# Kernel optimization log

Hardware: AMD Instinct MI355X
Metric: run time of the kernel (lower is better)

## Reference

```python
import jax, jax.numpy as jnp
import numpy as np

B, S, E, H = 2, 2048, 1024, 16
HD = E // H  # 64
NEG = -1e24


def setup_inputs() -> dict:
    key = jax.random.key(0)
    ks = jax.random.split(key, 20)
    sc_e = 1.0 / np.sqrt(E)
    inp = {
        "q_matrix": jax.random.normal(ks[0], (B, S, E), jnp.float32),
        "k_matrix": jax.random.normal(ks[1], (B, S, E), jnp.float32),
        "v_matrix": jax.random.normal(ks[2], (B, S, E), jnp.float32),
        "mask": jax.random.randint(ks[3], (B, S, S), 0, 2).astype(bool),
        # global QKV projections (embed_dim -> embed_dim)
        "Wq": jax.random.normal(ks[4], (E, E), jnp.float32) * sc_e,
        "bq": jnp.zeros((E,), jnp.float32),
        "Wk": jax.random.normal(ks[5], (E, E), jnp.float32) * sc_e,
        "bk": jnp.zeros((E,), jnp.float32),
        "Wv": jax.random.normal(ks[6], (E, E), jnp.float32) * sc_e,
        "bv": jnp.zeros((E,), jnp.float32),
        # per-head QKV projections (embed_dim -> head_dim), batched over heads
        "Whq": jax.random.normal(ks[7], (H, E, HD), jnp.float32) * sc_e,
        "bhq": jnp.zeros((H, HD), jnp.float32),
        "Whk": jax.random.normal(ks[8], (H, E, HD), jnp.float32) * sc_e,
        "bhk": jnp.zeros((H, HD), jnp.float32),
        "Whv": jax.random.normal(ks[9], (H, E, HD), jnp.float32) * sc_e,
        "bhv": jnp.zeros((H, HD), jnp.float32),
        # output projection
        "Wo": jax.random.normal(ks[10], (E, E), jnp.float32) * sc_e,
        "bo": jnp.zeros((E,), jnp.float32),
    }
    return inp


def reference(q_matrix, k_matrix, v_matrix, mask, Wq, bq, Wk, bk, Wv, bv,
              Whq, bhq, Whk, bhk, Whv, bhv, Wo, bo):
    # global projections [B,S,E]
    qg = q_matrix @ Wq + bq
    kg = k_matrix @ Wk + bk
    vg = v_matrix @ Wv + bv
    # per-head projections -> [B,H,S,HD]
    qh = jnp.einsum('bse,hed->bhsd', qg, Whq) + bhq[None, :, None, :]
    kh = jnp.einsum('bse,hed->bhsd', kg, Whk) + bhk[None, :, None, :]
    vh = jnp.einsum('bse,hed->bhsd', vg, Whv) + bhv[None, :, None, :]
    # scaled dot-product attention, scores [B,H,S,S]
    scores = jnp.einsum('bhsd,bhtd->bhst', qh, kh) / jnp.sqrt(jnp.float32(HD))
    scores = jnp.where(mask[:, None, :, :], NEG, scores)
    weights = jax.nn.softmax(scores, axis=-1)
    out = jnp.einsum('bhst,bhtd->bhsd', weights, vh)
    # concat heads (head order along last dim, matching torch.cat)
    x = out.transpose(0, 2, 1, 3).reshape(out.shape[0], out.shape[2], E)
    return x @ Wo + bo
```

## Files before the change

### kernel.cpp

```cpp
#include <hip/hip_runtime.h>
#include <hip/hip_bf16.h>

typedef unsigned short us16;
typedef __attribute__((ext_vector_type(8))) short short8;
typedef __attribute__((ext_vector_type(4))) float float4v;

#define E_DIM 1024
#define S_LEN 2048
#define B_DIM 2
#define H_DIM 16
#define HD_DIM 64
#define M_ROWS 4096
#define SCALE2 0.18033688011112042f

__device__ __forceinline__ float b2f(us16 b) {
    return __uint_as_float(((unsigned int)b) << 16);
}
__device__ __forceinline__ us16 f2b(float f) {
    unsigned int u = __float_as_uint(f);
    unsigned int r = (u + 0x7fffu + ((u >> 16) & 1u)) >> 16;
    return (us16)r;
}

__device__ __forceinline__ void gload16(const us16* g, us16* lds_uniform_base) {
    __builtin_amdgcn_global_load_lds(
        (const __attribute__((address_space(1))) void*)g,
        (__attribute__((address_space(3))) void*)lds_uniform_base, 16, 0, 0);
}

__global__ __launch_bounds__(256) void prep(
    const float* __restrict__ q, const float* __restrict__ k, const float* __restrict__ v,
    const float* __restrict__ Wq, const float* __restrict__ Wk, const float* __restrict__ Wv,
    const float* __restrict__ Whq, const float* __restrict__ Whk, const float* __restrict__ Whv,
    const float* __restrict__ Wo,
    const float* __restrict__ bq, const float* __restrict__ bk, const float* __restrict__ bv,
    const float* __restrict__ bhq, const float* __restrict__ bhk, const float* __restrict__ bhv,
    const int* __restrict__ mask,
    us16* qb, us16* kb, us16* vb, us16* Wqb, us16* Wkb, us16* Wvb,
    us16* WhqT, us16* WhkT, us16* WhvT, us16* WoT,
    us16* marr,
    float* bcq, float* bck, float* bcv, float* zbias)
{
    __shared__ us16 tile[32][33];
    __shared__ float red[4][64];
    int blk = blockIdx.x, tid = threadIdx.x;

    if (blk < 7680) {
        const float* in; us16* out; int idx;
        if (blk < 6144) {
            int z = blk >> 11, rem = blk & 2047;
            in = z == 0 ? q : z == 1 ? k : v;
            out = z == 0 ? qb : z == 1 ? kb : vb;
            idx = (rem * 256 + tid) * 8;
        } else {
            int t = blk - 6144, z = t >> 9, rem = t & 511;
            in = z == 0 ? Wq : z == 1 ? Wk : Wv;
            out = z == 0 ? Wqb : z == 1 ? Wkb : Wvb;
            idx = (rem * 256 + tid) * 8;
        }
        float4 f0 = *(const float4*)(in + idx);
        float4 f1 = *(const float4*)(in + idx + 4);
        us16 t8[8] = {f2b(f0.x), f2b(f0.y), f2b(f0.z), f2b(f0.w),
                      f2b(f1.x), f2b(f1.y), f2b(f1.z), f2b(f1.w)};
        *(uint4*)(out + idx) = *(const uint4*)t8;
    } else if (blk < 11776) {
        int t = blk - 7680, z = t >> 10, rem = t & 1023;
        const float* in = z == 0 ? Whq : z == 1 ? Whk : z == 2 ? Whv : Wo;
        us16* out = z == 0 ? WhqT : z == 1 ? WhkT : z == 2 ? WhvT : WoT;
        int mode = (z < 3) ? 1 : 0;
        int bx = rem & 31, by = rem >> 5;
        int tx = tid & 31, ty = tid >> 5;
#pragma unroll
        for (int i = 0; i < 4; ++i) {
            int e = by * 32 + ty + i * 8;
            int c = bx * 32 + tx;
            size_t src;
            if (mode == 0) src = (size_t)e * E_DIM + c;
            else           src = ((size_t)(c >> 6) * E_DIM + e) * 64 + (c & 63);
            tile[ty + i * 8][tx] = f2b(in[src]);
        }
        __syncthreads();
#pragma unroll
        for (int i = 0; i < 4; ++i) {
            int c = bx * 32 + ty + i * 8;
            int e = by * 32 + tx;
            out[(size_t)c * E_DIM + e] = tile[tx][ty + i * 8];
        }
    } else if (blk < 15872) {
        int g = (blk - 11776) * 256 + tid;
        int lane = g & 63, ld = (g >> 6) & 1, wv = (g >> 7) & 7;
        int q0t = (g >> 10) & 15, ktz = (g >> 14) & 31, bb = g >> 19;
        int quad = lane >> 4, l16 = lane & 15;
        int qq = q0t * 128 + wv * 16 + l16;
        int t0 = ktz * 64 + ld * 32 + quad * 4;
        const int* mp = mask + ((size_t)bb * S_LEN + qq) * S_LEN + t0;
        int4 ma = *(const int4*)mp;
        int4 mb2 = *(const int4*)(mp + 16);
        const us16 NEGB = f2b(-1e38f);
        us16 t8[8];
        t8[0] = ma.x ? NEGB : (us16)0;  t8[1] = ma.y ? NEGB : (us16)0;
        t8[2] = ma.z ? NEGB : (us16)0;  t8[3] = ma.w ? NEGB : (us16)0;
        t8[4] = mb2.x ? NEGB : (us16)0; t8[5] = mb2.y ? NEGB : (us16)0;
        t8[6] = mb2.z ? NEGB : (us16)0; t8[7] = mb2.w ? NEGB : (us16)0;
        *(uint4*)&marr[(size_t)g * 8] = *(const uint4*)t8;
    } else if (blk < 15920) {
        int t = blk - 15872, z = t >> 4, h = t & 15;
        const float* bg = z == 0 ? bq : z == 1 ? bk : bv;
        const float* Wh = z == 0 ? Whq : z == 1 ? Whk : Whv;
        const float* bh = z == 0 ? bhq : z == 1 ? bhk : bhv;
        float* bc = z == 0 ? bcq : z == 1 ? bck : bcv;
        float sc = (z == 0) ? SCALE2 : 1.0f;
        int d = tid & 63, part = tid >> 6;
        float acc = 0.f;
        int j0 = part * 256;
        for (int j = j0; j < j0 + 256; ++j)
            acc += bg[j] * Wh[((size_t)h * E_DIM + j) * HD_DIM + d];
        red[part][d] = acc;
        __syncthreads();
        if (tid < 64)
            bc[h * 64 + tid] = (red[0][tid] + red[1][tid] + red[2][tid] + red[3][tid] + bh[h * 64 + tid]) * sc;
    } else {
        int i = (blk - 15920) * 256 + tid;
        if (i < 1024) zbias[i] = 0.f;
    }
}

#define BK 32

__device__ __forceinline__ void gemm_body(
    const us16* __restrict__ A, const us16* __restrict__ Bt,
    const float* __restrict__ bias, void* __restrict__ Cp,
    int M, int N, int K, int bxt, int byt, int omode)
{
    __shared__ us16 As[128 * BK];
    __shared__ us16 Bs[128 * BK];

    int tid = threadIdx.x;
    int wave = tid >> 6, lane = tid & 63;
    int quad = lane >> 4, l16 = lane & 15;
    int wm = (wave >> 1) * 64, wn = (wave & 1) * 64;
    int bm0 = byt * 128, bn0 = bxt * 128;
    int srow = lane >> 2;
    int gcol = (((lane & 3) ^ (srow & 3)) << 3);
    int rslot = ((quad ^ (l16 & 3)) << 3);

    float4v acc[4][4];
#pragma unroll
    for (int i = 0; i < 4; ++i)
#pragma unroll
        for (int j = 0; j < 4; ++j)
#pragma unroll
            for (int r = 0; r < 4; ++r) acc[i][j][r] = 0.f;

    for (int k0 = 0; k0 < K; k0 += BK) {
#pragma unroll
        for (int c = 0; c < 2; ++c) {
            int r0 = 32 * wave + 16 * c;
            gload16(A  + (size_t)(bm0 + r0 + srow) * K + k0 + gcol, &As[r0 * BK]);
            gload16(Bt + (size_t)(bn0 + r0 + srow) * K + k0 + gcol, &Bs[r0 * BK]);
        }
        __syncthreads();
        short8 af[4], bfr[4];
#pragma unroll
        for (int i = 0; i < 4; ++i)
            af[i] = *(const short8*)&As[(wm + i * 16 + l16) * BK + rslot];
#pragma unroll
        for (int j = 0; j < 4; ++j)
            bfr[j] = *(const short8*)&Bs[(wn + j * 16 + l16) * BK + rslot];
#pragma unroll
        for (int i = 0; i < 4; ++i)
#pragma unroll
            for (int j = 0; j < 4; ++j)
                acc[i][j] = __builtin_amdgcn_mfma_f32_16x16x32_bf16(af[i], bfr[j], acc[i][j], 0, 0, 0);
        __syncthreads();
    }

#pragma unroll
    for (int i = 0; i < 4; ++i) {
#pragma unroll
        for (int j = 0; j < 4; ++j) {
#pragma unroll
            for (int r = 0; r < 4; ++r) {
                int row = bm0 + wm + i * 16 + quad * 4 + r;
                int col = bn0 + wn + j * 16 + l16;
                float vv = acc[i][j][r] + ((omode == 3) ? bias[row] : bias[col]);
                if (omode == 1) {
                    int b = row >> 11, s = row & 2047, h = col >> 6, d = col & 63;
                    ((us16*)Cp)[(((size_t)(b * H_DIM + h) * S_LEN + s) * HD_DIM) + d] = f2b(vv);
                } else {
                    int h = row >> 6, d = row & 63, b = col >> 11, sl = col & 2047;
                    ((us16*)Cp)[(((size_t)(b * H_DIM + h) * HD_DIM + d) * S_LEN) + sl] = f2b(vv);
                }
            }
        }
    }
}

__global__ __launch_bounds__(256) void proj_all(
    const us16* __restrict__ qb, const us16* __restrict__ kb, const us16* __restrict__ vb,
    const us16* __restrict__ WcqT, const us16* __restrict__ WckT, const us16* __restrict__ WcvT,
    const float* __restrict__ bcq, const float* __restrict__ bck, const float* __restrict__ bcv,
    us16* __restrict__ qhb, us16* __restrict__ khb, us16* __restrict__ vtb)
{
    int bx = blockIdx.x;
    int z = bx >> 8, t = bx & 255;
    if (z == 0)      gemm_body(qb, WcqT, bcq, qhb, M_ROWS, E_DIM, E_DIM, t & 7, t >> 3, 1);
    else if (z == 1) gemm_body(kb, WckT, bck, khb, M_ROWS, E_DIM, E_DIM, t & 7, t >> 3, 1);
    else             gemm_body(WcvT, vb, bcv, vtb, E_DIM, M_ROWS, E_DIM, t & 31, t >> 5, 3);
}

template<int OMODE>
__device__ __forceinline__ void gemm64_body(
    const us16* __restrict__ A, const us16* __restrict__ Bt,
    const float* __restrict__ bias, void* __restrict__ Cp,
    int M, int N, int K, int bxt, int byt, float oscale)
{
    __shared__ us16 As[64 * BK];
    __shared__ us16 Bs[128 * BK];

    int tid = threadIdx.x;
    int wave = tid >> 6, lane = tid & 63;
    int quad = lane >> 4, l16 = lane & 15;
    int wm = (wave >> 1) * 32, wn = (wave & 1) * 64;
    int bm0 = byt * 64, bn0 = bxt * 128;
    int srow = lane >> 2;
    int gcol = (((lane & 3) ^ (srow & 3)) << 3);
    int rslot = ((quad ^ (l16 & 3)) << 3);

    float4v acc[2][4];
#pragma unroll
    for (int i = 0; i < 2; ++i)
#pragma unroll
        for (int j = 0; j < 4; ++j)
#pragma unroll
            for (int r = 0; r < 4; ++r) acc[i][j][r] = 0.f;

    for (int k0 = 0; k0 < K; k0 += BK) {
        gload16(A + (size_t)(bm0 + 16 * wave + srow) * K + k0 + gcol, &As[16 * wave * BK]);
#pragma unroll
        for (int c = 0; c < 2; ++c) {
            int r0 = 32 * wave + 16 * c;
            gload16(Bt + (size_t)(bn0 + r0 + srow) * K + k0 + gcol, &Bs[r0 * BK]);
        }
        __syncthreads();
        short8 af[2], bfr[4];
#pragma unroll
        for (int i = 0; i < 2; ++i)
            af[i] = *(const short8*)&As[(wm + i * 16 + l16) * BK + rslot];
#pragma unroll
        for (int j = 0; j < 4; ++j)
            bfr[j] = *(const short8*)&Bs[(wn + j * 16 + l16) * BK + rslot];
#pragma unroll
        for (int i = 0; i < 2; ++i)
#pragma unroll
            for (int j = 0; j < 4; ++j)
                acc[i][j] = __builtin_amdgcn_mfma_f32_16x16x32_bf16(af[i], bfr[j], acc[i][j], 0, 0, 0);
        __syncthreads();
    }

#pragma unroll
    for (int i = 0; i < 2; ++i)
#pragma unroll
        for (int j = 0; j < 4; ++j)
#pragma unroll
            for (int r = 0; r < 4; ++r) {
                int row = bm0 + wm + i * 16 + quad * 4 + r;
                int col = bn0 + wn + j * 16 + l16;
                float vv = (acc[i][j][r] + bias[col]) * oscale;
                if (OMODE == 0) ((us16*)Cp)[(size_t)row * N + col] = f2b(vv);
                else            ((float*)Cp)[(size_t)row * N + col] = vv;
            }
}

__global__ __launch_bounds__(256) void wgemm3(
    const us16* A0, const us16* A1, const us16* A2,
    const us16* B0, const us16* B1, const us16* B2,
    const float* zbias, us16* C0, us16* C1, us16* C2)
{
    int z = blockIdx.z;
    const us16* A = z == 0 ? A0 : z == 1 ? A1 : A2;
    const us16* Bt = z == 0 ? B0 : z == 1 ? B1 : B2;
    us16* C = z == 0 ? C0 : z == 1 ? C1 : C2;
    float sc = (z == 0) ? SCALE2 : 1.0f;
    gemm64_body<0>(A, Bt, zbias, C, E_DIM, E_DIM, E_DIM, blockIdx.x, blockIdx.y, sc);
}

__global__ __launch_bounds__(256) void gemm_out64(
    const us16* __restrict__ A, const us16* __restrict__ Bt,
    const float* __restrict__ bias, float* __restrict__ C, int M, int N, int K)
{
    gemm64_body<2>(A, Bt, bias, C, M, N, K, blockIdx.x, blockIdx.y, 1.0f);
}

#define PST 72
#define NT 32

__global__ __launch_bounds__(512) void attn_kernel(
    const us16* __restrict__ qh, const us16* __restrict__ kh,
    const us16* __restrict__ vt, const us16* __restrict__ marr,
    us16* __restrict__ x)
{
    __shared__ us16 Ks[2][64 * 64];
    __shared__ us16 Vs[2][64 * 64];
    __shared__ us16 Pw[8][16 * PST];

    int tid = threadIdx.x;
    int w = tid >> 6, lane = tid & 63;
    int quad = lane >> 4, l16 = lane & 15;

    int wg = blockIdx.x;
    int xcd = wg & 7, idx = wg >> 3;
    int bh = xcd * 4 + (idx >> 4);
    int q0t = idx & 15;
    int q0 = q0t * 128;
    int b = bh >> 4;
    const size_t base = (size_t)bh * (S_LEN * HD_DIM);

    int qrow = q0 + w * 16 + l16;
    short8 qf0, qf1;
    {
        const us16* qp = qh + base + (size_t)qrow * HD_DIM + quad * 8;
        qf0 = *(const short8*)qp;
        qf1 = *(const short8*)(qp + 32);
    }

    short8 onesf;
#pragma unroll
    for (int j = 0; j < 8; ++j) onesf[j] = (short)0x3F80;

    int strow = w * 8 + (lane >> 3);
    int scol = ((lane & 7) ^ (strow & 7)) * 8;
    const us16* ksrc0 = kh + base + (size_t)strow * HD_DIM + scol;
    const us16* vsrc0 = vt + base + (size_t)strow * S_LEN + scol;

    const us16* mb0p = marr + ((((size_t)(b * 32) * 16 + q0t) * 8 + w) * 1024)
                            + (size_t)lane * 8;

    int slotA = (quad ^ (l16 & 7)) * 8;
    int slotB = slotA ^ 32;

    float4v o[4];
#pragma unroll
    for (int dt = 0; dt < 4; ++dt)
#pragma unroll
        for (int r = 0; r < 4; ++r) o[dt][r] = 0.f;
    float4v o_l;
#pragma unroll
    for (int r = 0; r < 4; ++r) o_l[r] = 0.f;

    auto QK = [&](const us16* KsC, uint4 m0, uint4 m1, float4v* sc) {
        __builtin_amdgcn_s_setprio(1);
#pragma unroll
        for (int ct = 0; ct < 4; ++ct) {
            int tt = ct * 16 + l16;
            short8 kf0 = *(const short8*)&KsC[tt * 64 + slotA];
            short8 kf1 = *(const short8*)&KsC[tt * 64 + slotB];
            unsigned w0, w1;
            if (ct == 0)      { w0 = m0.x; w1 = m0.y; }
            else if (ct == 1) { w0 = m0.z; w1 = m0.w; }
            else if (ct == 2) { w0 = m1.x; w1 = m1.y; }
            else              { w0 = m1.z; w1 = m1.w; }
            float4v a;
            a[0] = __uint_as_float(w0 << 16);
            a[1] = __uint_as_float(w0 & 0xFFFF0000u);
            a[2] = __uint_as_float(w1 << 16);
            a[3] = __uint_as_float(w1 & 0xFFFF0000u);
            a = __builtin_amdgcn_mfma_f32_16x16x32_bf16(kf0, qf0, a, 0, 0, 0);
            a = __builtin_amdgcn_mfma_f32_16x16x32_bf16(kf1, qf1, a, 0, 0, 0);
            sc[ct] = a;
        }
        __builtin_amdgcn_s_setprio(0);
    };

    gload16(ksrc0, &Ks[0][w * 512]);
    gload16(vsrc0, &Vs[0][w * 512]);
    gload16(ksrc0 + (size_t)64 * HD_DIM, &Ks[1][w * 512]);
    gload16(vsrc0 + 64, &Vs[1][w * 512]);
    uint4 mc0 = *(const uint4*)(mb0p);
    uint4 mc1 = *(const uint4*)(mb0p + 512);
    asm volatile("s_waitcnt vmcnt(2)" ::: "memory");
    __builtin_amdgcn_s_barrier();
    __builtin_amdgcn_sched_barrier(0);

    float4v sc[4];
    QK(Ks[0], mc0, mc1, sc);

    for (int t = 0; t < NT; ++t) {
        int cur = t & 1;

        uint4 mn0 = mc0, mn1 = mc1;
        if (t + 1 < NT) {
            const us16* mp = mb0p + (size_t)(t + 1) * 131072;
            mn0 = *(const uint4*)(mp);
            mn1 = *(const uint4*)(mp + 512);
        }

#pragma unroll
        for (int ct = 0; ct < 4; ++ct) {
            float p0 = __builtin_amdgcn_exp2f(sc[ct][0]);
            float p1 = __builtin_amdgcn_exp2f(sc[ct][1]);
            float p2 = __builtin_amdgcn_exp2f(sc[ct][2]);
            float p3 = __builtin_amdgcn_exp2f(sc[ct][3]);
            uint2 pk;
            asm("v_cvt_pk_bf16_f32 %0, %1, %2" : "=v"(pk.x) : "v"(p0), "v"(p1));
            asm("v_cvt_pk_bf16_f32 %0, %1, %2" : "=v"(pk.y) : "v"(p2), "v"(p3));
            *(uint2*)&Pw[w][l16 * PST + ct * 16 + quad * 4] = pk;
        }

        short8 pf0 = *(const short8*)&Pw[w][l16 * PST + quad * 8];
        short8 pf1 = *(const short8*)&Pw[w][l16 * PST + 32 + quad * 8];
        const us16* VsC = Vs[cur];
        __builtin_amdgcn_s_setprio(1);
#pragma unroll
        for (int dt = 0; dt < 4; ++dt) {
            int d = dt * 16 + l16;
            short8 vf0 = *(const short8*)&VsC[d * 64 + slotA];
            short8 vf1 = *(const short8*)&VsC[d * 64 + slotB];
            o[dt] = __builtin_amdgcn_mfma_f32_16x16x32_bf16(pf0, vf0, o[dt], 0, 0, 0);
            o[dt] = __builtin_amdgcn_mfma_f32_16x16x32_bf16(pf1, vf1, o[dt], 0, 0, 0);
        }
        o_l = __builtin_amdgcn_mfma_f32_16x16x32_bf16(pf0, onesf, o_l, 0, 0, 0);
        o_l = __builtin_amdgcn_mfma_f32_16x16x32_bf16(pf1, onesf, o_l, 0, 0, 0);
        __builtin_amdgcn_s_setprio(0);

        if (t + 1 == NT) break;

        __builtin_amdgcn_s_barrier();
        __builtin_amdgcn_sched_barrier(0);

        if (t + 2 < NT) {
            gload16(ksrc0 + (size_t)((t + 2) * 64) * HD_DIM, &Ks[cur][w * 512]);
            gload16(vsrc0 + (t + 2) * 64, &Vs[cur][w * 512]);
            asm volatile("s_waitcnt vmcnt(2)" ::: "memory");
        } else {
            asm volatile("s_waitcnt vmcnt(0)" ::: "memory");
        }
        __builtin_amdgcn_s_barrier();
        __builtin_amdgcn_sched_barrier(0);

        mc0 = mn0; mc1 = mn1;
        QK(Ks[cur ^ 1], mc0, mc1, sc);
    }

    float linv[4];
#pragma unroll
    for (int r = 0; r < 4; ++r) linv[r] = 1.0f / o_l[r];
    int h = bh & 15;
    int srow0 = q0 + w * 16 + quad * 4;
#pragma unroll
    for (int r = 0; r < 4; ++r) {
        size_t xro = ((size_t)(b * S_LEN + srow0 + r)) * E_DIM + h * HD_DIM;
#pragma unroll
        for (int dt = 0; dt < 4; ++dt)
            x[xro + dt * 16 + l16] = f2b(o[dt][r] * linv[r]);
    }
}

extern "C" void kernel_launch(void* const* d_in, const int* in_sizes, int n_in,
                              void* d_out, int out_size, void* d_ws, size_t ws_size,
                              hipStream_t stream) {
    const float* q    = (const float*)d_in[0];
    const float* k    = (const float*)d_in[1];
    const float* v    = (const float*)d_in[2];
    const int*   mask = (const int*)d_in[3];
    const float* Wq = (const float*)d_in[4];   const float* bq = (const float*)d_in[5];
    const float* Wk = (const float*)d_in[6];   const float* bk = (const float*)d_in[7];
    const float* Wv = (const float*)d_in[8];   const float* bv = (const float*)d_in[9];
    const float* Whq = (const float*)d_in[10]; const float* bhq = (const float*)d_in[11];
    const float* Whk = (const float*)d_in[12]; const float* bhk = (const float*)d_in[13];
    const float* Whv = (const float*)d_in[14]; const float* bhv = (const float*)d_in[15];
    const float* Wo = (const float*)d_in[16];  const float* bo = (const float*)d_in[17];

    us16* ws = (us16*)d_ws;
    const size_t M1 = (size_t)1 << 20;
    us16* WhqT = ws + 0 * M1;
    us16* WhkT = ws + 1 * M1;
    us16* WhvT = ws + 2 * M1;
    us16* WoT  = ws + 3 * M1;
    us16* WcqT = ws + 4 * M1;
    us16* WckT = ws + 5 * M1;
    us16* WcvT = ws + 6 * M1;
    us16* Wqb  = ws + 7 * M1;
    us16* Wkb  = ws + 8 * M1;
    us16* Wvb  = ws + 9 * M1;
    us16* qb   = ws + 10 * M1;
    us16* kb   = ws + 14 * M1;
    us16* vb   = ws + 18 * M1;
    us16* qhb  = ws + 22 * M1;
    us16* khb  = ws + 26 * M1;
    us16* vtb  = ws + 30 * M1;
    us16* xb   = vb;
    float* bcq   = (float*)(ws + 34 * M1);
    float* bck   = bcq + 1024;
    float* bcv   = bck + 1024;
    float* zbias = bcv + 1024;
    us16*  marr  = ws + 35 * M1;

    prep<<<15924, 256, 0, stream>>>(q, k, v, Wq, Wk, Wv, Whq, Whk, Whv, Wo,
                                    bq, bk, bv, bhq, bhk, bhv, mask,
                                    qb, kb, vb, Wqb, Wkb, Wvb,
                                    WhqT, WhkT, WhvT, WoT, marr,
                                    bcq, bck, bcv, zbias);

    wgemm3<<<dim3(8, 16, 3), 256, 0, stream>>>(WhqT, WhkT, WhvT, Wqb, Wkb, Wvb, zbias,
                                               WcqT, WckT, WcvT);

    proj_all<<<768, 256, 0, stream>>>(qb, kb, vb, WcqT, WckT, WcvT,
                                      bcq, bck, bcv, qhb, khb, vtb);

    attn_kernel<<<512, 512, 0, stream>>>(qhb, khb, vtb, marr, xb);

    gemm_out64<<<dim3(8, 64), 256, 0, stream>>>(xb, WoT, bo, (float*)d_out,
                                                M_ROWS, E_DIM, E_DIM);
}
```

Baseline: 298.3 us.

## Stage mask conversion through LDS for coalesced reads; use 128x128 GEMM tiles everywhere

The mask-to-bf16 conversion now reads 128x64 mask tiles row-contiguously into shared memory, then shuffles them into the MFMA-fragment layout before writing. The old version read scattered 16-byte pieces per lane directly from global memory. Separately, the 64-row GEMM body is removed, and the weight-combine and output-projection GEMMs now use the 128x128 tiled body, which halves their grids. Larger tiles give more reuse per block but fewer blocks for occupancy, and the prep kernel's shared-memory footprint grows.

```diff
diff --git a/kernel.cpp b/kernel.cpp
--- a/kernel.cpp
+++ b/kernel.cpp
@@ -43,6 +43,7 @@
 {
     __shared__ us16 tile[32][33];
     __shared__ float red[4][64];
+    __shared__ us16 Lm[128][72];
     int blk = blockIdx.x, tid = threadIdx.x;
 
     if (blk < 7680) {
@@ -86,25 +87,49 @@
             int e = by * 32 + tx;
             out[(size_t)c * E_DIM + e] = tile[tx][ty + i * 8];
         }
-    } else if (blk < 15872) {
-        int g = (blk - 11776) * 256 + tid;
-        int lane = g & 63, ld = (g >> 6) & 1, wv = (g >> 7) & 7;
-        int q0t = (g >> 10) & 15, ktz = (g >> 14) & 31, bb = g >> 19;
-        int quad = lane >> 4, l16 = lane & 15;
-        int qq = q0t * 128 + wv * 16 + l16;
-        int t0 = ktz * 64 + ld * 32 + quad * 4;
-        const int* mp = mask + ((size_t)bb * S_LEN + qq) * S_LEN + t0;
-        int4 ma = *(const int4*)mp;
-        int4 mb2 = *(const int4*)(mp + 16);
+    } else if (blk < 12032) {
+        int t2 = blk - 11776;
+        int ktg = t2 & 7, q0t2 = (t2 >> 3) & 15, bb = t2 >> 7;
         const us16 NEGB = f2b(-1e38f);
-        us16 t8[8];
-        t8[0] = ma.x ? NEGB : (us16)0;  t8[1] = ma.y ? NEGB : (us16)0;
-        t8[2] = ma.z ? NEGB : (us16)0;  t8[3] = ma.w ? NEGB : (us16)0;
-        t8[4] = mb2.x ? NEGB : (us16)0; t8[5] = mb2.y ? NEGB : (us16)0;
-        t8[6] = mb2.z ? NEGB : (us16)0; t8[7] = mb2.w ? NEGB : (us16)0;
-        *(uint4*)&marr[(size_t)g * 8] = *(const uint4*)t8;
-    } else if (blk < 15920) {
-        int t = blk - 15872, z = t >> 4, h = t & 15;
+        for (int kk = 0; kk < 4; ++kk) {
+            int kt = ktg * 4 + kk;
+            __syncthreads();
+#pragma unroll
+            for (int sgi = 0; sgi < 2; ++sgi) {
+                int seg = tid * 2 + sgi;
+                int row = seg >> 2, part = seg & 3;
+                const int* mp = mask + ((size_t)bb * S_LEN + q0t2 * 128 + row) * S_LEN
+                                + kt * 64 + part * 16;
+                us16 tmp[16];
+#pragma unroll
+                for (int gi = 0; gi < 4; ++gi) {
+                    int4 mv = *(const int4*)(mp + gi * 4);
+                    tmp[gi * 4 + 0] = mv.x ? NEGB : (us16)0;
+                    tmp[gi * 4 + 1] = mv.y ? NEGB : (us16)0;
+                    tmp[gi * 4 + 2] = mv.z ? NEGB : (us16)0;
+                    tmp[gi * 4 + 3] = mv.w ? NEGB : (us16)0;
+                }
+                *(uint4*)&Lm[row][part * 16]     = *(const uint4*)&tmp[0];
+                *(uint4*)&Lm[row][part * 16 + 8] = *(const uint4*)&tmp[8];
+            }
+            __syncthreads();
+            int wv2 = tid >> 5, ld2 = (tid >> 4) & 1, lb = (tid & 15) * 4;
+            us16 obuf[32];
+#pragma unroll
+            for (int li = 0; li < 4; ++li) {
+                int lane2 = lb + li;
+                int row = wv2 * 16 + (lane2 & 15);
+                int tb = ld2 * 32 + (lane2 >> 4) * 4;
+                *(uint2*)&obuf[li * 8]     = *(const uint2*)&Lm[row][tb];
+                *(uint2*)&obuf[li * 8 + 4] = *(const uint2*)&Lm[row][tb + 16];
+            }
+            size_t gbase = (((size_t)(bb * 32 + kt) * 16 + q0t2) * 8192) + (size_t)tid * 32;
+#pragma unroll
+            for (int gi = 0; gi < 4; ++gi)
+                *(uint4*)&marr[gbase + gi * 8] = *(const uint4*)&obuf[gi * 8];
+        }
+    } else if (blk < 12080) {
+        int t = blk - 12032, z = t >> 4, h = t & 15;
         const float* bg = z == 0 ? bq : z == 1 ? bk : bv;
         const float* Wh = z == 0 ? Whq : z == 1 ? Whk : Whv;
         const float* bh = z == 0 ? bhq : z == 1 ? bhk : bhv;
@@ -120,7 +145,7 @@
         if (tid < 64)
             bc[h * 64 + tid] = (red[0][tid] + red[1][tid] + red[2][tid] + red[3][tid] + bh[h * 64 + tid]) * sc;
     } else {
-        int i = (blk - 15920) * 256 + tid;
+        int i = (blk - 12080) * 256 + tid;
         if (i < 1024) zbias[i] = 0.f;
     }
 }
@@ -130,7 +155,7 @@
 __device__ __forceinline__ void gemm_body(
     const us16* __restrict__ A, const us16* __restrict__ Bt,
     const float* __restrict__ bias, void* __restrict__ Cp,
-    int M, int N, int K, int bxt, int byt, int omode)
+    int M, int N, int K, int bxt, int byt, int omode, float oscale)
 {
     __shared__ us16 As[128 * BK];
     __shared__ us16 Bs[128 * BK];
@@ -184,9 +209,13 @@
                 int row = bm0 + wm + i * 16 + quad * 4 + r;
                 int col = bn0 + wn + j * 16 + l16;
                 float vv = acc[i][j][r] + ((omode == 3) ? bias[row] : bias[col]);
-                if (omode == 1) {
+                if (omode == 0) {
+                    ((us16*)Cp)[(size_t)row * N + col] = f2b(vv * oscale);
+                } else if (omode == 1) {
                     int b = row >> 11, s = row & 2047, h = col >> 6, d = col & 63;
                     ((us16*)Cp)[(((size_t)(b * H_DIM + h) * S_LEN + s) * HD_DIM) + d] = f2b(vv);
+                } else if (omode == 2) {
+                    ((float*)Cp)[(size_t)row * N + col] = vv;
                 } else {
                     int h = row >> 6, d = row & 63, b = col >> 11, sl = col & 2047;
                     ((us16*)Cp)[(((size_t)(b * H_DIM + h) * HD_DIM + d) * S_LEN) + sl] = f2b(vv);
@@ -204,72 +233,9 @@
 {
     int bx = blockIdx.x;
     int z = bx >> 8, t = bx & 255;
-    if (z == 0)      gemm_body(qb, WcqT, bcq, qhb, M_ROWS, E_DIM, E_DIM, t & 7, t >> 3, 1);
-    else if (z == 1) gemm_body(kb, WckT, bck, khb, M_ROWS, E_DIM, E_DIM, t & 7, t >> 3, 1);
-    else             gemm_body(WcvT, vb, bcv, vtb, E_DIM, M_ROWS, E_DIM, t & 31, t >> 5, 3);
-}
-
-template<int OMODE>
-__device__ __forceinline__ void gemm64_body(
-    const us16* __restrict__ A, const us16* __restrict__ Bt,
-    const float* __restrict__ bias, void* __restrict__ Cp,
-    int M, int N, int K, int bxt, int byt, float oscale)
-{
-    __shared__ us16 As[64 * BK];
-    __shared__ us16 Bs[128 * BK];
-
-    int tid = threadIdx.x;
-    int wave = tid >> 6, lane = tid & 63;
-    int quad = lane >> 4, l16 = lane & 15;
-    int wm = (wave >> 1) * 32, wn = (wave & 1) * 64;
-    int bm0 = byt * 64, bn0 = bxt * 128;
-    int srow = lane >> 2;
-    int gcol = (((lane & 3) ^ (srow & 3)) << 3);
-    int rslot = ((quad ^ (l16 & 3)) << 3);
-
-    float4v acc[2][4];
-#pragma unroll
-    for (int i = 0; i < 2; ++i)
-#pragma unroll
-        for (int j = 0; j < 4; ++j)
-#pragma unroll
-            for (int r = 0; r < 4; ++r) acc[i][j][r] = 0.f;
-
-    for (int k0 = 0; k0 < K; k0 += BK) {
-        gload16(A + (size_t)(bm0 + 16 * wave + srow) * K + k0 + gcol, &As[16 * wave * BK]);
-#pragma unroll
-        for (int c = 0; c < 2; ++c) {
-            int r0 = 32 * wave + 16 * c;
-            gload16(Bt + (size_t)(bn0 + r0 + srow) * K + k0 + gcol, &Bs[r0 * BK]);
-        }
-        __syncthreads();
-        short8 af[2], bfr[4];
-#pragma unroll
-        for (int i = 0; i < 2; ++i)
-            af[i] = *(const short8*)&As[(wm + i * 16 + l16) * BK + rslot];
-#pragma unroll
-        for (int j = 0; j < 4; ++j)
-            bfr[j] = *(const short8*)&Bs[(wn + j * 16 + l16) * BK + rslot];
-#pragma unroll
-        for (int i = 0; i < 2; ++i)
-#pragma unroll
-            for (int j = 0; j < 4; ++j)
-                acc[i][j] = __builtin_amdgcn_mfma_f32_16x16x32_bf16(af[i], bfr[j], acc[i][j], 0, 0, 0);
-        __syncthreads();
-    }
-
-#pragma unroll
-    for (int i = 0; i < 2; ++i)
-#pragma unroll
-        for (int j = 0; j < 4; ++j)
-#pragma unroll
-            for (int r = 0; r < 4; ++r) {
-                int row = bm0 + wm + i * 16 + quad * 4 + r;
-                int col = bn0 + wn + j * 16 + l16;
-                float vv = (acc[i][j][r] + bias[col]) * oscale;
-                if (OMODE == 0) ((us16*)Cp)[(size_t)row * N + col] = f2b(vv);
-                else            ((float*)Cp)[(size_t)row * N + col] = vv;
-            }
+    if (z == 0)      gemm_body(qb, WcqT, bcq, qhb, M_ROWS, E_DIM, E_DIM, t & 7, t >> 3, 1, 1.0f);
+    else if (z == 1) gemm_body(kb, WckT, bck, khb, M_ROWS, E_DIM, E_DIM, t & 7, t >> 3, 1, 1.0f);
+    else             gemm_body(WcvT, vb, bcv, vtb, E_DIM, M_ROWS, E_DIM, t & 31, t >> 5, 3, 1.0f);
 }
 
 __global__ __launch_bounds__(256) void wgemm3(
@@ -282,14 +248,14 @@
     const us16* Bt = z == 0 ? B0 : z == 1 ? B1 : B2;
     us16* C = z == 0 ? C0 : z == 1 ? C1 : C2;
     float sc = (z == 0) ? SCALE2 : 1.0f;
-    gemm64_body<0>(A, Bt, zbias, C, E_DIM, E_DIM, E_DIM, blockIdx.x, blockIdx.y, sc);
-}
-
-__global__ __launch_bounds__(256) void gemm_out64(
+    gemm_body(A, Bt, zbias, C, E_DIM, E_DIM, E_DIM, blockIdx.x, blockIdx.y, 0, sc);
+}
+
+__global__ __launch_bounds__(256) void gemm_out(
     const us16* __restrict__ A, const us16* __restrict__ Bt,
     const float* __restrict__ bias, float* __restrict__ C, int M, int N, int K)
 {
-    gemm64_body<2>(A, Bt, bias, C, M, N, K, blockIdx.x, blockIdx.y, 1.0f);
+    gemm_body(A, Bt, bias, C, M, N, K, blockIdx.x, blockIdx.y, 2, 1.0f);
 }
 
 #define PST 72
@@ -496,20 +462,20 @@
     float* zbias = bcv + 1024;
     us16*  marr  = ws + 35 * M1;
 
-    prep<<<15924, 256, 0, stream>>>(q, k, v, Wq, Wk, Wv, Whq, Whk, Whv, Wo,
+    prep<<<12084, 256, 0, stream>>>(q, k, v, Wq, Wk, Wv, Whq, Whk, Whv, Wo,
                                     bq, bk, bv, bhq, bhk, bhv, mask,
                                     qb, kb, vb, Wqb, Wkb, Wvb,
                                     WhqT, WhkT, WhvT, WoT, marr,
                                     bcq, bck, bcv, zbias);
 
-    wgemm3<<<dim3(8, 16, 3), 256, 0, stream>>>(WhqT, WhkT, WhvT, Wqb, Wkb, Wvb, zbias,
-                                               WcqT, WckT, WcvT);
+    wgemm3<<<dim3(8, 8, 3), 256, 0, stream>>>(WhqT, WhkT, WhvT, Wqb, Wkb, Wvb, zbias,
+                                              WcqT, WckT, WcvT);
 
     proj_all<<<768, 256, 0, stream>>>(qb, kb, vb, WcqT, WckT, WcvT,
                                       bcq, bck, bcv, qhb, khb, vtb);
 
     attn_kernel<<<512, 512, 0, stream>>>(qhb, khb, vtb, marr, xb);
 
-    gemm_out64<<<dim3(8, 64), 256, 0, stream>>>(xb, WoT, bo, (float*)d_out,
-                                                M_ROWS, E_DIM, E_DIM);
-}
+    gemm_out<<<dim3(8, 32), 256, 0, stream>>>(xb, WoT, bo, (float*)d_out,
+                                              M_ROWS, E_DIM, E_DIM);
+}
```

Measured after the change: 343.0 us. +15.0%, slower.
